# Kernel tuning notes

Hardware: AMD Instinct MI355X
Metric: run time of the kernel (lower is better)

## Reference

```python
import jax, jax.numpy as jnp
import numpy as np


def setup_inputs() -> dict:
    key = jax.random.key(0)
    k1, k2 = jax.random.split(key)
    N, DIM = 32768, 1024
    M, K, D = 8, 1024, 128  # n_quantizer, n_codeword, sub_dim
    x = jax.random.normal(k1, (N, DIM), dtype=jnp.float32)
    CodeBooks = jax.random.uniform(k2, (M, K, D), dtype=jnp.float32)  # torch.rand init
    return {"x": x, "CodeBooks": CodeBooks, "soft_rate": -1}


def reference(x, CodeBooks, soft_rate):
    # x: [N, dim]; CodeBooks: [M, K, D] with dim = M*D
    N = x.shape[0]
    M, K, D = CodeBooks.shape
    # forward detaches x before quantizing
    sx = jax.lax.stop_gradient(x).reshape(-1, M, D)  # [N, M, D]
    # squared euclidean distances for all sub-quantizers at once:
    # d2[n,m,k] = ||sx[n,m] - CB[m,k]||^2
    dots = jnp.einsum("nmd,mkd->nmk", sx, CodeBooks)          # [N, M, K]
    x2 = jnp.sum(sx * sx, axis=-1)                             # [N, M]
    c2 = jnp.sum(CodeBooks * CodeBooks, axis=-1)               # [M, K]
    d2 = x2[:, :, None] + c2[None, :, :] - 2.0 * dots          # [N, M, K]
    if soft_rate == -1:
        # argmax of -dist == argmin of squared dist (sqrt is monotone)
        idx = jnp.argmin(d2, axis=-1)                          # [N, M]
        Q = CodeBooks[jnp.arange(M)[None, :], idx]             # [N, M, D]
    else:
        dist = -jnp.sqrt(jnp.maximum(d2, 0.0))                 # -cdist, p=2
        w = jax.nn.softmax(dist * soft_rate, axis=-1)          # [N, M, K]
        Q = jnp.einsum("nmk,mkd->nmd", w, CodeBooks)           # [N, M, D]
    return Q.reshape(N, M * D)
```

## Files before the change

kernel.cpp:

```cpp
#include <hip/hip_runtime.h>
#include <stdint.h>

#define NROWS   32768
#define XDIM    1024
#define NCB     8
#define NCODE   1024
#define CDIM    128

#define CHUNK   32
#define NCHUNK  (NCODE / CHUNK)

#define NTH     512
#define ROWS_PB 256
#define RPW     32

typedef _Float16 h8 __attribute__((ext_vector_type(8)));
typedef float    f4 __attribute__((ext_vector_type(4)));

#define LO_SCALE 2048.0f
#define LO_INV   4.8828125e-4f

#define BLOB_BYTES 16384
#define WS_C2   ((size_t)NCB * NCHUNK * BLOB_BYTES)
#define WS_NEED (WS_C2 + (size_t)NCB * NCODE * 4)

__device__ __forceinline__ void gload_lds16(const void* g, void* l) {
    __builtin_amdgcn_global_load_lds(
        (const __attribute__((address_space(1))) void*)g,
        (__attribute__((address_space(3))) void*)l, 16, 0, 0);
}

__global__ __launch_bounds__(256)
void precompute_kernel(const float* __restrict__ cb, uint8_t* __restrict__ ws)
{
    float* c2 = (float*)(ws + WS_C2);

    const int idx  = blockIdx.x * 256 + threadIdx.x;
    const int g    = idx & 15;
    const int code = idx >> 4;
    const int mm   = code >> 10;
    const int c    = (code & 1023) >> 5;
    const int k    = code & 31;

    const float* src = cb + (size_t)code * CDIM + g * 8;
    float v[8];
    *(f4*)&v[0] = *(const f4*)src;
    *(f4*)&v[4] = *(const f4*)(src + 4);

    _Float16 hh[8], ll[8];
    double s = 0.0;
    #pragma unroll
    for (int i = 0; i < 8; ++i) {
        _Float16 h = (_Float16)v[i];
        float    r = v[i] - (float)h;
        hh[i] = h; ll[i] = (_Float16)(r * LO_SCALE);
        s = fma((double)v[i], (double)v[i], s);
    }
    uint8_t* blob = ws + ((size_t)(mm * NCHUNK + c)) * BLOB_BYTES;
    *(h8*)(blob + g * 512 + k * 16)        = *(h8*)hh;
    *(h8*)(blob + 8192 + g * 512 + k * 16) = *(h8*)ll;

    #pragma unroll
    for (int mask = 1; mask <= 8; mask <<= 1)
        s += __shfl_xor(s, mask, 16);
    if (g == 0) c2[code] = (float)s;
}

__global__ __launch_bounds__(NTH, 4)
void quant_fast(const float* __restrict__ x, const float* __restrict__ cb,
                const uint8_t* __restrict__ ws, float* __restrict__ out)
{
    __shared__ __align__(16) _Float16 S[2][2][16][CHUNK][8];
    __shared__ float  c2s[NCODE];
    __shared__ float  x2s[ROWS_PB];
    __shared__ int    idxs[ROWS_PB];

    const float* c2w = (const float*)(ws + WS_C2);

    const int t    = threadIdx.x;
    const int m    = blockIdx.x & 7;
    const int rb   = blockIdx.x >> 3;
    const int row0 = rb * ROWS_PB;

    const int l    = t & 63;
    const int w    = t >> 6;
    const int l15  = l & 15;
    const int lh   = l >> 4;

    auto stage = [&](int c, int buf) {
        const uint8_t* src = ws + ((size_t)(m * NCHUNK + c) << 14) + (w << 11) + (l << 4);
        char* dst = (char*)&S[0][0][0][0][0] + buf * 16384 + (w << 11);
        gload_lds16(src,        dst);
        gload_lds16(src + 1024, dst + 1024);
    };

    stage(0, 0);

    if (t < 256) *(f4*)&c2s[t * 4] = *(const f4*)&c2w[m * NCODE + t * 4];

    h8 xh[2][4], xl[2][4];
    #pragma unroll
    for (int rs = 0; rs < 2; ++rs) {
        const float* xp = x + (size_t)(row0 + w * RPW + rs * 16 + l15) * XDIM + m * CDIM + lh * 8;
        double s = 0.0;
        #pragma unroll
        for (int ks = 0; ks < 4; ++ks) {
            float v[8];
            *(f4*)&v[0] = *(const f4*)(xp + ks * 32);
            *(f4*)&v[4] = *(const f4*)(xp + ks * 32 + 4);
            #pragma unroll
            for (int i = 0; i < 8; ++i) {
                _Float16 h = (_Float16)v[i];
                float    r = v[i] - (float)h;
                xh[rs][ks][i] = h;
                xl[rs][ks][i] = (_Float16)(r * LO_SCALE);
                s = fma((double)v[i], (double)v[i], s);
            }
        }
        s += __shfl_xor(s, 16, 64);
        s += __shfl_xor(s, 32, 64);
        if (lh == 0) x2s[w * RPW + rs * 16 + l15] = (float)s;
    }

    __syncthreads();

    float x2r[2][4];
    #pragma unroll
    for (int rs = 0; rs < 2; ++rs)
        #pragma unroll
        for (int j = 0; j < 4; ++j)
            x2r[rs][j] = x2s[w * RPW + rs * 16 + lh * 4 + j];

    float mval[2][4];
    int   midx[2][4];
    #pragma unroll
    for (int rs = 0; rs < 2; ++rs)
        #pragma unroll
        for (int j = 0; j < 4; ++j) { mval[rs][j] = 3.0e38f; midx[rs][j] = 0; }

    const _Float16* Sl = &S[0][0][0][0][0] + (lh * 256 + l15 * 8);

    for (int c = 0; c < NCHUNK; ++c) {
        const int cur = c & 1;
        if (c + 1 < NCHUNK) stage(c + 1, cur ^ 1);

        const _Float16* Sc = Sl + cur * 8192;

        #pragma unroll
        for (int cf = 0; cf < 2; ++cf) {
            f4 accH[2] = {{0,0,0,0},{0,0,0,0}};
            f4 accS[2] = {{0,0,0,0},{0,0,0,0}};

            h8 bh = *(const h8*)(Sc +        cf * 128);
            h8 bl = *(const h8*)(Sc + 4096 + cf * 128);
            #pragma unroll
            for (int ks = 0; ks < 4; ++ks) {
                h8 bhn, bln;
                if (ks < 3) {
                    bhn = *(const h8*)(Sc +        (ks + 1) * 1024 + cf * 128);
                    bln = *(const h8*)(Sc + 4096 + (ks + 1) * 1024 + cf * 128);
                } else { bhn = bh; bln = bl; }
                accH[0] = __builtin_amdgcn_mfma_f32_16x16x32_f16(xh[0][ks], bh, accH[0], 0, 0, 0);
                accH[1] = __builtin_amdgcn_mfma_f32_16x16x32_f16(xh[1][ks], bh, accH[1], 0, 0, 0);
                accS[0] = __builtin_amdgcn_mfma_f32_16x16x32_f16(xh[0][ks], bl, accS[0], 0, 0, 0);
                accS[0] = __builtin_amdgcn_mfma_f32_16x16x32_f16(xl[0][ks], bh, accS[0], 0, 0, 0);
                accS[1] = __builtin_amdgcn_mfma_f32_16x16x32_f16(xh[1][ks], bl, accS[1], 0, 0, 0);
                accS[1] = __builtin_amdgcn_mfma_f32_16x16x32_f16(xl[1][ks], bh, accS[1], 0, 0, 0);
                asm volatile("" ::: "memory");
                bh = bhn; bl = bln;
            }
            const int   code = c * CHUNK + cf * 16 + l15;
            const float c2v  = c2s[code];
            #pragma unroll
            for (int rs = 0; rs < 2; ++rs)
                #pragma unroll
                for (int j = 0; j < 4; ++j) {
                    float dot = fmaf(accS[rs][j], LO_INV, accH[rs][j]);
                    float d2  = (x2r[rs][j] + c2v) - 2.0f * dot;
                    if (d2 < mval[rs][j]) { mval[rs][j] = d2; midx[rs][j] = code; }
                }
        }
        __syncthreads();
    }

    #pragma unroll
    for (int mask = 1; mask <= 8; mask <<= 1)
        #pragma unroll
        for (int rs = 0; rs < 2; ++rs)
            #pragma unroll
            for (int j = 0; j < 4; ++j) {
                float ov = __shfl_xor(mval[rs][j], mask, 64);
                int   oi = __shfl_xor(midx[rs][j], mask, 64);
                if (ov < mval[rs][j] || (ov == mval[rs][j] && oi < midx[rs][j])) {
                    mval[rs][j] = ov; midx[rs][j] = oi;
                }
            }
    if (l15 == 0)
        #pragma unroll
        for (int rs = 0; rs < 2; ++rs)
            #pragma unroll
            for (int j = 0; j < 4; ++j)
                idxs[w * RPW + rs * 16 + lh * 4 + j] = midx[rs][j];
    __syncthreads();

    {
        const int row  = t >> 1;
        const int half = (t & 1) * 64;
        const float* src = cb + ((size_t)m * NCODE + idxs[row]) * CDIM + half;
        float*       dst = out + (size_t)(row0 + row) * XDIM + m * CDIM + half;
        #pragma unroll
        for (int i = 0; i < 16; ++i)
            *(f4*)(dst + i * 4) = *(const f4*)(src + i * 4);
    }
}

__global__ __launch_bounds__(512, 4)
void quant_fallback(const float* __restrict__ x, const float* __restrict__ cb,
                    float* __restrict__ out)
{
    __shared__ __align__(16) _Float16 chS[2][CHUNK][CDIM];
    __shared__ __align__(16) _Float16 clS[2][CHUNK][CDIM];
    __shared__ float  c2s[NCODE];
    __shared__ double x2p[4][128];
    __shared__ float  x2s[128];
    __shared__ int    idxs[128];

    const int t = threadIdx.x, bid = blockIdx.x;
    const int m = bid >> 8, rb = bid & 255, row0 = rb * 128;
    const int l = t & 63, w = t >> 6, l15 = l & 15, lh = l >> 4;
    const int mskr = (l & 7) * 8;

    for (int rep = 0; rep < 2; ++rep) {
        int k = t + rep * 512;
        const float* p = cb + ((size_t)m * NCODE + k) * CDIM;
        double s0 = 0, s1 = 0, s2 = 0, s3 = 0;
        for (int d = 0; d < CDIM; d += 4) {
            double v0 = p[d], v1 = p[d+1], v2 = p[d+2], v3 = p[d+3];
            s0 = fma(v0,v0,s0); s1 = fma(v1,v1,s1); s2 = fma(v2,v2,s2); s3 = fma(v3,v3,s3);
        }
        c2s[k] = (float)((s0+s1)+(s2+s3));
    }
    {
        int row = t >> 2, q = t & 3;
        const float* p = x + (size_t)(row0+row)*XDIM + m*CDIM + q*32;
        double s0 = 0, s1 = 0;
        for (int i = 0; i < 32; i += 2) { double v0=p[i], v1=p[i+1]; s0=fma(v0,v0,s0); s1=fma(v1,v1,s1); }
        x2p[q][row] = s0 + s1;
    }
    h8 xh[4], xl[4];
    {
        const float* xp = x + (size_t)(row0 + w*16 + l15)*XDIM + m*CDIM + lh*8;
        #pragma unroll
        for (int ks = 0; ks < 4; ++ks) {
            float v[8];
            *(f4*)&v[0] = *(const f4*)(xp + ks*32);
            *(f4*)&v[4] = *(const f4*)(xp + ks*32 + 4);
            #pragma unroll
            for (int i = 0; i < 8; ++i) {
                _Float16 h = (_Float16)v[i]; float r = v[i] - (float)h;
                xh[ks][i] = h; xl[ks][i] = (_Float16)(r * LO_SCALE);
            }
        }
    }
    __syncthreads();
    if (t < 128) x2s[t] = (float)((x2p[0][t]+x2p[1][t])+(x2p[2][t]+x2p[3][t]));

    const int kr = t >> 4, db = (t & 15) * 8, ew = db ^ ((kr & 7) * 8);
    auto stage_load = [&](int c, f4& a, f4& b) {
        const float* p = cb + ((size_t)m*NCODE + c*CHUNK + kr)*CDIM + db;
        a = *(const f4*)p; b = *(const f4*)(p + 4);
    };
    auto stage_write = [&](int buf, f4 a, f4 b) {
        float v[8]; *(f4*)&v[0] = a; *(f4*)&v[4] = b;
        _Float16 hh[8], ll[8];
        #pragma unroll
        for (int i = 0; i < 8; ++i) {
            _Float16 h = (_Float16)v[i]; float r = v[i] - (float)h;
            hh[i] = h; ll[i] = (_Float16)(r * LO_SCALE);
        }
        *(h8*)&chS[buf][kr][ew] = *(h8*)hh;
        *(h8*)&clS[buf][kr][ew] = *(h8*)ll;
    };

    f4 pa, pb;
    stage_load(0, pa, pb);
    stage_write(0, pa, pb);
    __syncthreads();

    float x2r[4];
    #pragma unroll
    for (int j = 0; j < 4; ++j) x2r[j] = x2s[w*16 + lh*4 + j];
    float mval[4]; int midx[4];
    #pragma unroll
    for (int j = 0; j < 4; ++j) { mval[j] = 3.0e38f; midx[j] = 0; }

    for (int c = 0; c < NCHUNK; ++c) {
        const int cur = c & 1;
        f4 na, nb;
        if (c + 1 < NCHUNK) stage_load(c + 1, na, nb);
        #pragma unroll
        for (int cf = 0; cf < 2; ++cf) {
            const int kloc = cf*16 + l15;
            f4 accH = {0,0,0,0}, accS = {0,0,0,0};
            #pragma unroll
            for (int ks = 0; ks < 4; ++ks) {
                const int e = (ks*32 + lh*8) ^ mskr;
                h8 bh = *(const h8*)&chS[cur][kloc][e];
                h8 bl = *(const h8*)&clS[cur][kloc][e];
                accH = __builtin_amdgcn_mfma_f32_16x16x32_f16(xh[ks], bh, accH, 0, 0, 0);
                accS = __builtin_amdgcn_mfma_f32_16x16x32_f16(xh[ks], bl, accS, 0, 0, 0);
                accS = __builtin_amdgcn_mfma_f32_16x16x32_f16(xl[ks], bh, accS, 0, 0, 0);
            }
            const int code = c*CHUNK + kloc;
            const float c2v = c2s[code];
            #pragma unroll
            for (int j = 0; j < 4; ++j) {
                float dot = fmaf(accS[j], LO_INV, accH[j]);
                float d2 = (x2r[j] + c2v) - 2.0f*dot;
                if (d2 < mval[j]) { mval[j] = d2; midx[j] = code; }
            }
        }
        if (c + 1 < NCHUNK) stage_write((c + 1) & 1, na, nb);
        __syncthreads();
    }
    #pragma unroll
    for (int mask = 1; mask <= 8; mask <<= 1)
        #pragma unroll
        for (int j = 0; j < 4; ++j) {
            float ov = __shfl_xor(mval[j], mask, 64);
            int   oi = __shfl_xor(midx[j], mask, 64);
            if (ov < mval[j] || (ov == mval[j] && oi < midx[j])) { mval[j] = ov; midx[j] = oi; }
        }
    if (l15 == 0)
        #pragma unroll
        for (int j = 0; j < 4; ++j) idxs[w*16 + lh*4 + j] = midx[j];
    __syncthreads();
    {
        const int row = t >> 2, qd = (t & 3) * 32;
        const float* src = cb + ((size_t)m*NCODE + idxs[row])*CDIM + qd;
        float* dst = out + (size_t)(row0+row)*XDIM + m*CDIM + qd;
        #pragma unroll
        for (int i = 0; i < 8; ++i) *(f4*)(dst + i*4) = *(const f4*)(src + i*4);
    }
}

extern "C" void kernel_launch(void* const* d_in, const int* in_sizes, int n_in,
                              void* d_out, int out_size, void* d_ws, size_t ws_size,
                              hipStream_t stream) {
    const float* x   = (const float*)d_in[0];
    const float* cb  = (const float*)d_in[1];
    float*       out = (float*)d_out;
    if (ws_size >= WS_NEED && d_ws != nullptr) {
        precompute_kernel<<<dim3(512), dim3(256), 0, stream>>>(cb, (uint8_t*)d_ws);
        quant_fast<<<dim3(NCB * (NROWS / ROWS_PB)), dim3(NTH), 0, stream>>>(
            x, cb, (const uint8_t*)d_ws, out);
    } else {
        quant_fallback<<<dim3(2048), dim3(512), 0, stream>>>(x, cb, out);
    }
}
```

Measured before the change: 366.3 us.

## Read codebook fragments directly from global memory instead of LDS double buffering

Removes the LDS double-buffered staging of codebook chunks and the per-chunk block barrier, so each wave loads its B fragments straight from the preformatted global workspace (through L1/L2) into registers before the MFMA sequence. This drops LDS traffic and __syncthreads stalls and lets waves run independently. In exchange, every wave re-fetches the same codebook data from cache, global-load latency is exposed with no explicit prefetch across chunks, and register pressure rises.

```diff
diff --git a/kernel.cpp b/kernel.cpp
--- a/kernel.cpp
+++ b/kernel.cpp
@@ -70,7 +70,6 @@
 void quant_fast(const float* __restrict__ x, const float* __restrict__ cb,
                 const uint8_t* __restrict__ ws, float* __restrict__ out)
 {
-    __shared__ __align__(16) _Float16 S[2][2][16][CHUNK][8];
     __shared__ float  c2s[NCODE];
     __shared__ float  x2s[ROWS_PB];
     __shared__ int    idxs[ROWS_PB];
@@ -86,15 +85,6 @@
     const int w    = t >> 6;
     const int l15  = l & 15;
     const int lh   = l >> 4;
-
-    auto stage = [&](int c, int buf) {
-        const uint8_t* src = ws + ((size_t)(m * NCHUNK + c) << 14) + (w << 11) + (l << 4);
-        char* dst = (char*)&S[0][0][0][0][0] + buf * 16384 + (w << 11);
-        gload_lds16(src,        dst);
-        gload_lds16(src + 1024, dst + 1024);
-    };
-
-    stage(0, 0);
 
     if (t < 256) *(f4*)&c2s[t * 4] = *(const f4*)&c2w[m * NCODE + t * 4];
 
@@ -138,36 +128,31 @@
         #pragma unroll
         for (int j = 0; j < 4; ++j) { mval[rs][j] = 3.0e38f; midx[rs][j] = 0; }
 
-    const _Float16* Sl = &S[0][0][0][0][0] + (lh * 256 + l15 * 8);
-
+    const uint8_t* mbase = ws + (size_t)m * NCHUNK * BLOB_BYTES;
+    const int      loff  = lh * 512 + l15 * 16;
+
+    #pragma unroll 1
     for (int c = 0; c < NCHUNK; ++c) {
-        const int cur = c & 1;
-        if (c + 1 < NCHUNK) stage(c + 1, cur ^ 1);
-
-        const _Float16* Sc = Sl + cur * 8192;
+        const uint8_t* B0 = mbase + c * BLOB_BYTES + loff;
 
         #pragma unroll
         for (int cf = 0; cf < 2; ++cf) {
+            h8 bh[4], bl[4];
+            #pragma unroll
+            for (int ks = 0; ks < 4; ++ks) {
+                bh[ks] = *(const h8*)(B0 + ks * 2048 + cf * 256);
+                bl[ks] = *(const h8*)(B0 + 8192 + ks * 2048 + cf * 256);
+            }
             f4 accH[2] = {{0,0,0,0},{0,0,0,0}};
             f4 accS[2] = {{0,0,0,0},{0,0,0,0}};
-
-            h8 bh = *(const h8*)(Sc +        cf * 128);
-            h8 bl = *(const h8*)(Sc + 4096 + cf * 128);
             #pragma unroll
             for (int ks = 0; ks < 4; ++ks) {
-                h8 bhn, bln;
-                if (ks < 3) {
-                    bhn = *(const h8*)(Sc +        (ks + 1) * 1024 + cf * 128);
-                    bln = *(const h8*)(Sc + 4096 + (ks + 1) * 1024 + cf * 128);
-                } else { bhn = bh; bln = bl; }
-                accH[0] = __builtin_amdgcn_mfma_f32_16x16x32_f16(xh[0][ks], bh, accH[0], 0, 0, 0);
-                accH[1] = __builtin_amdgcn_mfma_f32_16x16x32_f16(xh[1][ks], bh, accH[1], 0, 0, 0);
-                accS[0] = __builtin_amdgcn_mfma_f32_16x16x32_f16(xh[0][ks], bl, accS[0], 0, 0, 0);
-                accS[0] = __builtin_amdgcn_mfma_f32_16x16x32_f16(xl[0][ks], bh, accS[0], 0, 0, 0);
-                accS[1] = __builtin_amdgcn_mfma_f32_16x16x32_f16(xh[1][ks], bl, accS[1], 0, 0, 0);
-                accS[1] = __builtin_amdgcn_mfma_f32_16x16x32_f16(xl[1][ks], bh, accS[1], 0, 0, 0);
-                asm volatile("" ::: "memory");
-                bh = bhn; bl = bln;
+                accH[0] = __builtin_amdgcn_mfma_f32_16x16x32_f16(xh[0][ks], bh[ks], accH[0], 0, 0, 0);
+                accH[1] = __builtin_amdgcn_mfma_f32_16x16x32_f16(xh[1][ks], bh[ks], accH[1], 0, 0, 0);
+                accS[0] = __builtin_amdgcn_mfma_f32_16x16x32_f16(xh[0][ks], bl[ks], accS[0], 0, 0, 0);
+                accS[0] = __builtin_amdgcn_mfma_f32_16x16x32_f16(xl[0][ks], bh[ks], accS[0], 0, 0, 0);
+                accS[1] = __builtin_amdgcn_mfma_f32_16x16x32_f16(xh[1][ks], bl[ks], accS[1], 0, 0, 0);
+                accS[1] = __builtin_amdgcn_mfma_f32_16x16x32_f16(xl[1][ks], bh[ks], accS[1], 0, 0, 0);
             }
             const int   code = c * CHUNK + cf * 16 + l15;
             const float c2v  = c2s[code];
@@ -179,8 +164,8 @@
                     float d2  = (x2r[rs][j] + c2v) - 2.0f * dot;
                     if (d2 < mval[rs][j]) { mval[rs][j] = d2; midx[rs][j] = code; }
                 }
-        }
-        __syncthreads();
+            asm volatile("" ::: "memory");
+        }
     }
 
     #pragma unroll
```

Result: slower. 460.5 us (+25.7%).
